# Performance work log

Hardware: AMD Instinct MI355X
Metric: run time of the kernel (lower is better)

## Reference

```python
import jax, jax.numpy as jnp
import numpy as np

B, L, D = 16, 1024, 512   # batch, input_seq_len, d_model
H, DH = 8, 64             # ac_heads, d_model // ac_heads (= d_v)
C_FACTOR = 2              # config['c']


def setup_inputs() -> dict:
    key = jax.random.key(0)
    ks = jax.random.split(key, 5)
    Q = jax.random.normal(ks[0], (B, L, D), jnp.float32)
    K = jax.random.normal(ks[1], (B, L, D), jnp.float32)
    V = jax.random.normal(ks[2], (B, L, D), jnp.float32)
    Wq = jax.random.normal(ks[3], (D, DH), jnp.float32) * (1.0 / np.sqrt(D))
    bq = jax.random.normal(ks[4], (DH,), jnp.float32) * 0.02
    return {"Q": Q, "K": K, "V": V, "Wq": Wq, "bq": bq}


def reference(Q, K, V, Wq, bq):
    B_, L_, D_ = Q.shape
    dh = Wq.shape[1]
    heads = D_ // dh
    # The source reuses self.query for Q, K and V projections (keys/values
    # Dense layers are dead code), so one shared (Wq, bq) is faithful.
    q = Q @ Wq + bq   # [B, L, dh]
    k_ = K @ Wq + bq
    v = V @ Wq + bq
    # Source stacks `heads` identical copies of the same projection, then
    # transposes to [B, H, dh, L]; broadcast instead of recomputing.
    to_heads = lambda x: jnp.broadcast_to(
        jnp.swapaxes(x, 1, 2)[:, None], (B_, heads, dh, L_))
    qh = to_heads(q).astype(jnp.complex64)
    kh = to_heads(k_).astype(jnp.complex64)
    vh = to_heads(v)
    # FFT-based circular cross-correlation along the time axis
    corr = jnp.real(jnp.fft.ifft(jnp.fft.fft(qh) * jnp.conj(jnp.fft.fft(kh))))  # [B,H,dh,L]
    ktop = int(C_FACTOR * np.log(L_))
    vals, idxs = jax.lax.top_k(corr, ktop)          # [B,H,dh,k]
    w = jax.nn.softmax(vals, axis=-1)               # softmax over the k lags
    # tf.roll(v, shift=-idx)[j] == v[(j + idx) mod L]: one gather per lag
    pos = (idxs[..., None] + jnp.arange(L_)) % L_    # [B,H,dh,k,L]
    vg = jnp.take_along_axis(vh[..., None, :], pos, axis=-1)  # [B,H,dh,k,L]
    agg = jnp.sum(w[..., None] * vg, axis=-2)        # [B,H,dh,L]
    # reshape to [B, d_model, L] then transpose -> [B, L, d_model]
    return jnp.swapaxes(agg.reshape(B_, heads * dh, L_), 1, 2)
```

## Files before the change

kernel.cpp:

```cpp
#include <hip/hip_runtime.h>
#include <float.h>
#include <math.h>

#define PROJ_N (16*64*1024)

__global__ __launch_bounds__(256) void proj_kernel(
    const float* __restrict__ Q, const float* __restrict__ K,
    const float* __restrict__ V, const float* __restrict__ Wq,
    const float* __restrict__ bq, float* __restrict__ proj) {
  __shared__ float XsT[64 * 64];
  __shared__ float Ws[64 * 64];

  const int blk  = blockIdx.x;
  const int in   = blk >> 8;
  const int row0 = (blk & 255) << 6;
  const float* __restrict__ X = (in == 0) ? Q : (in == 1 ? K : V);

  const int t  = threadIdx.x;
  const int c4 = t & 15;
  const int rr = t >> 4;
  const int tx = t & 15;
  const int ty = t >> 4;

  float acc[4][4] = {{0.f,0.f,0.f,0.f},{0.f,0.f,0.f,0.f},
                     {0.f,0.f,0.f,0.f},{0.f,0.f,0.f,0.f}};

  for (int kt = 0; kt < 8; ++kt) {
    const int k0 = kt << 6;
    __syncthreads();

#pragma unroll
    for (int it = 0; it < 4; ++it) {
      const int r = it * 16 + rr;
      float4 f = *(const float4*)&X[(size_t)(row0 + r) * 512 + k0 + 4 * c4];
      const int sw = ((((r >> 2) ^ (c4 & 7)) << 2) | (r & 3));
      XsT[(4 * c4 + 0) * 64 + sw] = f.x;
      XsT[(4 * c4 + 1) * 64 + sw] = f.y;
      XsT[(4 * c4 + 2) * 64 + sw] = f.z;
      XsT[(4 * c4 + 3) * 64 + sw] = f.w;
      float4 g = *(const float4*)&Wq[(size_t)(k0 + r) * 64 + 4 * c4];
      *(float4*)&Ws[r * 64 + 4 * c4] = g;
    }
    __syncthreads();

#pragma unroll 4
    for (int kk = 0; kk < 64; ++kk) {
      const int sk = (kk >> 2) & 7;
      float4 x4 = *(float4*)&XsT[kk * 64 + ((ty ^ sk) << 2)];
      float4 wv = *(float4*)&Ws[kk * 64 + 4 * tx];
      acc[0][0] += x4.x * wv.x; acc[0][1] += x4.x * wv.y;
      acc[0][2] += x4.x * wv.z; acc[0][3] += x4.x * wv.w;
      acc[1][0] += x4.y * wv.x; acc[1][1] += x4.y * wv.y;
      acc[1][2] += x4.y * wv.z; acc[1][3] += x4.y * wv.w;
      acc[2][0] += x4.z * wv.x; acc[2][1] += x4.z * wv.y;
      acc[2][2] += x4.z * wv.z; acc[2][3] += x4.z * wv.w;
      acc[3][0] += x4.w * wv.x; acc[3][1] += x4.w * wv.y;
      acc[3][2] += x4.w * wv.z; acc[3][3] += x4.w * wv.w;
    }
  }

  const int b  = row0 >> 10;
  const int l0 = row0 & 1023;
  float* __restrict__ op = proj + (size_t)in * PROJ_N + (size_t)(b * 64) * 1024;
#pragma unroll
  for (int j = 0; j < 4; ++j) {
    const int d = 4 * tx + j;
    const float bias = bq[d];
    float4 o = make_float4(acc[0][j] + bias, acc[1][j] + bias,
                           acc[2][j] + bias, acc[3][j] + bias);
    *(float4*)&op[(size_t)d * 1024 + l0 + 4 * ty] = o;
  }
}

__global__ __launch_bounds__(128) void corr_topk_kernel(
    const float* __restrict__ qp, const float* __restrict__ kp,
    float* __restrict__ wvals, int* __restrict__ widx) {
  __shared__ float qs[1024];
  __shared__ float ks8[2048];
  __shared__ float tv[13];
  __shared__ int   ts[13];
  __shared__ float rwv[2];
  __shared__ int   rws[2];
  __shared__ int   bsh;

  const int pair = blockIdx.x;
  const int t = threadIdx.x;
  const float* __restrict__ qg = qp + (size_t)pair * 1024;
  const float* __restrict__ kg = kp + (size_t)pair * 1024;

  *(float4*)&qs[4 * t]         = *(const float4*)&qg[4 * t];
  *(float4*)&qs[4 * (t + 128)] = *(const float4*)&qg[4 * (t + 128)];
#pragma unroll
  for (int jj = 0; jj < 4; ++jj) {
    const int j = t + jj * 128;
    float4 f = *(const float4*)&kg[(4 * j) & 1023];
    const int e = j & 1, c2 = j >> 1;
    ks8[(0 * 2 + e) * 256 + c2] = f.x;
    ks8[(1 * 2 + e) * 256 + c2] = f.y;
    ks8[(2 * 2 + e) * 256 + c2] = f.z;
    ks8[(3 * 2 + e) * 256 + c2] = f.w;
  }
  __syncthreads();

  float w[11];
  const int Bt = 1017 - 8 * t;
#pragma unroll
  for (int m = 0; m < 11; ++m) {
    const int g = Bt + m;
    w[m] = ks8[(((g & 3) << 1) | ((g >> 2) & 1)) * 256 + (g >> 3)];
  }

  float acc[8] = {0.f,0.f,0.f,0.f,0.f,0.f,0.f,0.f};
#pragma unroll 4
  for (int lc = 0; lc < 255; ++lc) {
    float4 q4 = *(float4*)&qs[4 * lc];
#pragma unroll
    for (int i = 0; i < 8; ++i)
      acc[i] += q4.x * w[7 - i] + q4.y * w[8 - i] + q4.z * w[9 - i] + q4.w * w[10 - i];
#pragma unroll
    for (int m = 0; m < 7; ++m) w[m] = w[m + 4];
    const int c = lc + 257 - 2 * t;
    const int base = ((c & 1) << 8) + (c >> 1);
    w[7]  = ks8[base];
    w[8]  = ks8[512 + base];
    w[9]  = ks8[1024 + base];
    w[10] = ks8[1536 + base];
  }
  {
    float4 q4 = *(float4*)&qs[4 * 255];
#pragma unroll
    for (int i = 0; i < 8; ++i)
      acc[i] += q4.x * w[7 - i] + q4.y * w[8 - i] + q4.z * w[9 - i] + q4.w * w[10 - i];
  }

  for (int r = 0; r < 13; ++r) {
    float m = acc[0]; int mi = 0;
#pragma unroll
    for (int i = 1; i < 8; ++i)
      if (acc[i] > m) { m = acc[i]; mi = i; }
    int ms = 8 * t + mi;
#pragma unroll
    for (int off = 32; off >= 1; off >>= 1) {
      float om = __shfl_xor(m, off, 64);
      int   os = __shfl_xor(ms, off, 64);
      if (om > m || (om == m && os < ms)) { m = om; ms = os; }
    }
    if ((t & 63) == 0) { rwv[t >> 6] = m; rws[t >> 6] = ms; }
    __syncthreads();
    if (t == 0) {
      float bv = rwv[0]; int bs = rws[0];
      if (rwv[1] > bv || (rwv[1] == bv && rws[1] < bs)) { bv = rwv[1]; bs = rws[1]; }
      tv[r] = bv; ts[r] = bs; bsh = bs;
    }
    __syncthreads();
    const int bs = bsh;
    if ((bs >> 3) == t) acc[bs & 7] = -FLT_MAX;
  }

  if (t == 0) {
    const float mx = tv[0];
    float e[13]; float s = 0.f;
#pragma unroll
    for (int k = 0; k < 13; ++k) { e[k] = __expf(tv[k] - mx); s += e[k]; }
    const float inv = 1.f / s;
#pragma unroll
    for (int k = 0; k < 13; ++k) {
      wvals[pair * 16 + k] = e[k] * inv;
      widx [pair * 16 + k] = ts[k];
    }
  }
}

__global__ __launch_bounds__(256) void agg_kernel(
    const float* __restrict__ vp, const float* __restrict__ wvals,
    const int* __restrict__ widx, float* __restrict__ agg) {
  __shared__ float vs[2048];
  __shared__ float wv[13];
  __shared__ int   wi[13];
  const int pair = blockIdx.x;
  const int t = threadIdx.x;
  const float* __restrict__ vg = vp + (size_t)pair * 1024;
  *(float4*)&vs[4 * t]         = *(const float4*)&vg[(4 * t) & 1023];
  *(float4*)&vs[4 * (t + 256)] = *(const float4*)&vg[(4 * (t + 256)) & 1023];
  if (t < 13) { wv[t] = wvals[pair * 16 + t]; wi[t] = widx[pair * 16 + t]; }
  __syncthreads();

  float r0 = 0.f, r1 = 0.f, r2 = 0.f, r3 = 0.f;
#pragma unroll
  for (int k = 0; k < 13; ++k) {
    const float wk = wv[k];
    const int   ik = wi[k];
    r0 += wk * vs[t        + ik];
    r1 += wk * vs[t + 256  + ik];
    r2 += wk * vs[t + 512  + ik];
    r3 += wk * vs[t + 768  + ik];
  }
  float* __restrict__ ag = agg + (size_t)pair * 1024;
  ag[t] = r0; ag[t + 256] = r1; ag[t + 512] = r2; ag[t + 768] = r3;
}

__global__ __launch_bounds__(256) void out_kernel(
    const float* __restrict__ agg, float* __restrict__ out) {
  __shared__ float tile[64][65];
  const int blk = blockIdx.x;
  const int b = blk >> 4, lt = blk & 15;
  const int l0 = lt * 64;
  const int t = threadIdx.x;
  const int j = t & 63, qq = t >> 6;

#pragma unroll
  for (int p = 0; p < 16; ++p) {
    const int d = p * 4 + qq;
    tile[d][j] = agg[(size_t)(b * 64 + d) * 1024 + l0 + j];
  }
  __syncthreads();
#pragma unroll
  for (int p = 0; p < 16; ++p) {
    const int jj = p * 4 + qq;
    const float val = tile[j][jj];
    const size_t rowbase = ((size_t)(b * 1024 + l0 + jj)) * 512;
#pragma unroll
    for (int h = 0; h < 8; ++h)
      out[rowbase + h * 64 + j] = val;
  }
}

extern "C" void kernel_launch(void* const* d_in, const int* in_sizes, int n_in,
                              void* d_out, int out_size, void* d_ws, size_t ws_size,
                              hipStream_t stream) {
  const float* Q  = (const float*)d_in[0];
  const float* K  = (const float*)d_in[1];
  const float* V  = (const float*)d_in[2];
  const float* Wq = (const float*)d_in[3];
  const float* bq = (const float*)d_in[4];
  float* out = (float*)d_out;
  float* ws  = (float*)d_ws;

  float* proj  = ws;
  float* agg   = ws + (size_t)3 * PROJ_N;
  float* wvals = ws + (size_t)4 * PROJ_N;
  int*   widx  = (int*)(ws + (size_t)4 * PROJ_N + 16384);

  proj_kernel<<<768, 256, 0, stream>>>(Q, K, V, Wq, bq, proj);
  corr_topk_kernel<<<1024, 128, 0, stream>>>(proj, proj + PROJ_N, wvals, widx);
  agg_kernel<<<1024, 256, 0, stream>>>(proj + (size_t)2 * PROJ_N, wvals, widx, agg);
  out_kernel<<<256, 256, 0, stream>>>(agg, out);
}
```

Before: 220.2 us.

## Compute circular correlation with split-bf16 MFMA Toeplitz matmul

Replaces the scalar FP32 circular cross-correlation with a matrix-core formulation. Each 32x32 output tile is a Toeplitz product built from shifted K and Q slices, computed with bf16 MFMA using a hi/lo split (three products) to approximate FP32 accuracy. Partial results from four waves are reduced through shared memory, and top-k then runs over 256 threads. The split-bf16 scheme drops the lo*lo term, so near-tied correlation values could select different top-k indices than FP32.

Result: faster. 188.7 us (-14.3%).

```diff
diff --git a/kernel.cpp b/kernel.cpp
--- a/kernel.cpp
+++ b/kernel.cpp
@@ -3,6 +3,10 @@
 #include <math.h>
 
 #define PROJ_N (16*64*1024)
+
+using short8_t  = __attribute__((ext_vector_type(8)))  short;
+using uint4_t   = __attribute__((ext_vector_type(4)))  unsigned;
+using floatx16  = __attribute__((ext_vector_type(16))) float;
 
 __global__ __launch_bounds__(256) void proj_kernel(
     const float* __restrict__ Q, const float* __restrict__ K,
@@ -28,7 +32,6 @@
   for (int kt = 0; kt < 8; ++kt) {
     const int k0 = kt << 6;
     __syncthreads();
-
 #pragma unroll
     for (int it = 0; it < 4; ++it) {
       const int r = it * 16 + rr;
@@ -72,92 +75,152 @@
   }
 }
 
-__global__ __launch_bounds__(128) void corr_topk_kernel(
+__device__ __forceinline__ unsigned bf16r(float x) {
+  unsigned u = __float_as_uint(x);
+  return (u + 0x7FFFu + ((u >> 16) & 1u)) >> 16;
+}
+__device__ __forceinline__ unsigned pk_bf16(float x, float y) {
+  return bf16r(x) | (bf16r(y) << 16);
+}
+
+__global__ __launch_bounds__(256) void corr_mfma_kernel(
     const float* __restrict__ qp, const float* __restrict__ kp,
     float* __restrict__ wvals, int* __restrict__ widx) {
-  __shared__ float qs[1024];
-  __shared__ float ks8[2048];
+  __shared__ __align__(16) short qh[2048];
+  __shared__ __align__(16) short ql[2048];
+  __shared__ __align__(16) short kh[2048];
+  __shared__ __align__(16) short kl[2048];
+  __shared__ float corr4[4][1024];
   __shared__ float tv[13];
   __shared__ int   ts[13];
-  __shared__ float rwv[2];
-  __shared__ int   rws[2];
+  __shared__ float rv[4];
+  __shared__ int   rs[4];
   __shared__ int   bsh;
 
   const int pair = blockIdx.x;
-  const int t = threadIdx.x;
+  const int tid  = threadIdx.x;
+  const int w    = tid >> 6;
+  const int lane = tid & 63;
+  const int row  = lane & 31;
+  const int hk   = lane >> 5;
+
   const float* __restrict__ qg = qp + (size_t)pair * 1024;
   const float* __restrict__ kg = kp + (size_t)pair * 1024;
 
-  *(float4*)&qs[4 * t]         = *(const float4*)&qg[4 * t];
-  *(float4*)&qs[4 * (t + 128)] = *(const float4*)&qg[4 * (t + 128)];
-#pragma unroll
-  for (int jj = 0; jj < 4; ++jj) {
-    const int j = t + jj * 128;
-    float4 f = *(const float4*)&kg[(4 * j) & 1023];
-    const int e = j & 1, c2 = j >> 1;
-    ks8[(0 * 2 + e) * 256 + c2] = f.x;
-    ks8[(1 * 2 + e) * 256 + c2] = f.y;
-    ks8[(2 * 2 + e) * 256 + c2] = f.z;
-    ks8[(3 * 2 + e) * 256 + c2] = f.w;
+  {
+    const int j = (tid << 3) & 1023;
+    float4 a0 = *(const float4*)&qg[j];
+    float4 a1 = *(const float4*)&qg[j + 4];
+    float fq[8] = {a0.x, a0.y, a0.z, a0.w, a1.x, a1.y, a1.z, a1.w};
+    unsigned hb[8]; float lf[8];
+#pragma unroll
+    for (int m = 0; m < 8; ++m) {
+      hb[m] = bf16r(fq[m]);
+      lf[m] = fq[m] - __uint_as_float(hb[m] << 16);
+    }
+    uint4_t vqh = { hb[0] | (hb[1] << 16), hb[2] | (hb[3] << 16),
+                    hb[4] | (hb[5] << 16), hb[6] | (hb[7] << 16) };
+    uint4_t vql = { pk_bf16(lf[0], lf[1]), pk_bf16(lf[2], lf[3]),
+                    pk_bf16(lf[4], lf[5]), pk_bf16(lf[6], lf[7]) };
+    *(uint4_t*)&qh[tid << 3] = vqh;
+    *(uint4_t*)&ql[tid << 3] = vql;
+
+    float4 b0 = *(const float4*)&kg[j];
+    float4 b1 = *(const float4*)&kg[j + 4];
+    float fk[8] = {b0.x, b0.y, b0.z, b0.w, b1.x, b1.y, b1.z, b1.w};
+#pragma unroll
+    for (int m = 0; m < 8; ++m) {
+      hb[m] = bf16r(fk[m]);
+      lf[m] = fk[m] - __uint_as_float(hb[m] << 16);
+    }
+    uint4_t vkh = { hb[0] | (hb[1] << 16), hb[2] | (hb[3] << 16),
+                    hb[4] | (hb[5] << 16), hb[6] | (hb[7] << 16) };
+    uint4_t vkl = { pk_bf16(lf[0], lf[1]), pk_bf16(lf[2], lf[3]),
+                    pk_bf16(lf[4], lf[5]), pk_bf16(lf[6], lf[7]) };
+    const int p = tid ^ ((tid >> 3) & 7);
+    *(uint4_t*)&kh[p << 3] = vkh;
+    *(uint4_t*)&kl[p << 3] = vkl;
   }
   __syncthreads();
 
-  float w[11];
-  const int Bt = 1017 - 8 * t;
-#pragma unroll
-  for (int m = 0; m < 11; ++m) {
-    const int g = Bt + m;
-    w[m] = ks8[(((g & 3) << 1) | ((g >> 2) & 1)) * 256 + (g >> 3)];
-  }
-
-  float acc[8] = {0.f,0.f,0.f,0.f,0.f,0.f,0.f,0.f};
-#pragma unroll 4
-  for (int lc = 0; lc < 255; ++lc) {
-    float4 q4 = *(float4*)&qs[4 * lc];
-#pragma unroll
-    for (int i = 0; i < 8; ++i)
-      acc[i] += q4.x * w[7 - i] + q4.y * w[8 - i] + q4.z * w[9 - i] + q4.w * w[10 - i];
-#pragma unroll
-    for (int m = 0; m < 7; ++m) w[m] = w[m + 4];
-    const int c = lc + 257 - 2 * t;
-    const int base = ((c & 1) << 8) + (c >> 1);
-    w[7]  = ks8[base];
-    w[8]  = ks8[512 + base];
-    w[9]  = ks8[1024 + base];
-    w[10] = ks8[1536 + base];
-  }
-  {
-    float4 q4 = *(float4*)&qs[4 * 255];
-#pragma unroll
-    for (int i = 0; i < 8; ++i)
-      acc[i] += q4.x * w[7 - i] + q4.y * w[8 - i] + q4.z * w[9 - i] + q4.w * w[10 - i];
-  }
+  floatx16 acc = {0.f,0.f,0.f,0.f,0.f,0.f,0.f,0.f,
+                  0.f,0.f,0.f,0.f,0.f,0.f,0.f,0.f};
+  const unsigned* __restrict__ qhd = (const unsigned*)qh;
+  const unsigned* __restrict__ qld = (const unsigned*)ql;
+#pragma unroll
+  for (int i = 0; i < 16; ++i) {
+    const int k0 = (w << 8) + (i << 4);
+    const int e0 = 1024 + k0 + (hk << 3) - (row << 5);
+    const int c  = e0 >> 3;
+    const int p  = c ^ ((c >> 3) & 7);
+    short8_t ah = *(const short8_t*)&kh[p << 3];
+    short8_t al = *(const short8_t*)&kl[p << 3];
+    const int s0 = k0 + (hk << 3) + row;
+    const int d0 = s0 >> 1;
+    const unsigned sh = (s0 & 1) << 4;
+    unsigned w0 = qhd[d0 + 0], w1 = qhd[d0 + 1], w2 = qhd[d0 + 2],
+             w3 = qhd[d0 + 3], w4 = qhd[d0 + 4];
+    uint4_t buh = { __builtin_amdgcn_alignbit(w1, w0, sh),
+                    __builtin_amdgcn_alignbit(w2, w1, sh),
+                    __builtin_amdgcn_alignbit(w3, w2, sh),
+                    __builtin_amdgcn_alignbit(w4, w3, sh) };
+    unsigned x0 = qld[d0 + 0], x1 = qld[d0 + 1], x2 = qld[d0 + 2],
+             x3 = qld[d0 + 3], x4 = qld[d0 + 4];
+    uint4_t bul = { __builtin_amdgcn_alignbit(x1, x0, sh),
+                    __builtin_amdgcn_alignbit(x2, x1, sh),
+                    __builtin_amdgcn_alignbit(x3, x2, sh),
+                    __builtin_amdgcn_alignbit(x4, x3, sh) };
+    short8_t bh = __builtin_bit_cast(short8_t, buh);
+    short8_t bl = __builtin_bit_cast(short8_t, bul);
+    acc = __builtin_amdgcn_mfma_f32_32x32x16_bf16(ah, bh, acc, 0, 0, 0);
+    acc = __builtin_amdgcn_mfma_f32_32x32x16_bf16(ah, bl, acc, 0, 0, 0);
+    acc = __builtin_amdgcn_mfma_f32_32x32x16_bf16(al, bh, acc, 0, 0, 0);
+  }
+
+#pragma unroll
+  for (int r = 0; r < 16; ++r) {
+    const int srow = (r & 3) + ((r >> 2) << 3) + (hk << 2);
+    corr4[w][(srow << 5) | row] = acc[r];
+  }
+  __syncthreads();
+
+  float v0 = corr4[0][tid]       + corr4[1][tid]       + corr4[2][tid]       + corr4[3][tid];
+  float v1 = corr4[0][tid + 256] + corr4[1][tid + 256] + corr4[2][tid + 256] + corr4[3][tid + 256];
+  float v2 = corr4[0][tid + 512] + corr4[1][tid + 512] + corr4[2][tid + 512] + corr4[3][tid + 512];
+  float v3 = corr4[0][tid + 768] + corr4[1][tid + 768] + corr4[2][tid + 768] + corr4[3][tid + 768];
 
   for (int r = 0; r < 13; ++r) {
-    float m = acc[0]; int mi = 0;
-#pragma unroll
-    for (int i = 1; i < 8; ++i)
-      if (acc[i] > m) { m = acc[i]; mi = i; }
-    int ms = 8 * t + mi;
+    float bv = v0; int bs = tid;
+    if (v1 > bv) { bv = v1; bs = tid + 256; }
+    if (v2 > bv) { bv = v2; bs = tid + 512; }
+    if (v3 > bv) { bv = v3; bs = tid + 768; }
 #pragma unroll
     for (int off = 32; off >= 1; off >>= 1) {
-      float om = __shfl_xor(m, off, 64);
-      int   os = __shfl_xor(ms, off, 64);
-      if (om > m || (om == m && os < ms)) { m = om; ms = os; }
-    }
-    if ((t & 63) == 0) { rwv[t >> 6] = m; rws[t >> 6] = ms; }
+      float ov = __shfl_xor(bv, off, 64);
+      int   os = __shfl_xor(bs, off, 64);
+      if (ov > bv || (ov == bv && os < bs)) { bv = ov; bs = os; }
+    }
+    if (lane == 0) { rv[w] = bv; rs[w] = bs; }
     __syncthreads();
-    if (t == 0) {
-      float bv = rwv[0]; int bs = rws[0];
-      if (rwv[1] > bv || (rwv[1] == bv && rws[1] < bs)) { bv = rwv[1]; bs = rws[1]; }
-      tv[r] = bv; ts[r] = bs; bsh = bs;
+    if (tid == 0) {
+      float cv = rv[0]; int cs = rs[0];
+#pragma unroll
+      for (int u = 1; u < 4; ++u)
+        if (rv[u] > cv || (rv[u] == cv && rs[u] < cs)) { cv = rv[u]; cs = rs[u]; }
+      tv[r] = cv; ts[r] = cs; bsh = cs;
     }
     __syncthreads();
-    const int bs = bsh;
-    if ((bs >> 3) == t) acc[bs & 7] = -FLT_MAX;
-  }
-
-  if (t == 0) {
+    const int bw = bsh;
+    if ((bw & 255) == tid) {
+      const int slot = bw >> 8;
+      if      (slot == 0) v0 = -FLT_MAX;
+      else if (slot == 1) v1 = -FLT_MAX;
+      else if (slot == 2) v2 = -FLT_MAX;
+      else                v3 = -FLT_MAX;
+    }
+  }
+
+  if (tid == 0) {
     const float mx = tv[0];
     float e[13]; float s = 0.f;
 #pragma unroll
@@ -242,7 +305,7 @@
   int*   widx  = (int*)(ws + (size_t)4 * PROJ_N + 16384);
 
   proj_kernel<<<768, 256, 0, stream>>>(Q, K, V, Wq, bq, proj);
-  corr_topk_kernel<<<1024, 128, 0, stream>>>(proj, proj + PROJ_N, wvals, widx);
+  corr_mfma_kernel<<<1024, 256, 0, stream>>>(proj, proj + PROJ_N, wvals, widx);
   agg_kernel<<<1024, 256, 0, stream>>>(proj + (size_t)2 * PROJ_N, wvals, widx, agg);
   out_kernel<<<256, 256, 0, stream>>>(agg, out);
 }
```
